# Optimization experiments

Hardware: AMD Instinct MI355X
Metric: run time of the kernel (lower is better)

## Reference

```python
import jax, jax.numpy as jnp
import numpy as np

B = 256          # batch
IMG = 28         # img_width
K = 9            # kernel_size
NUM_CLASSES = 10
NUM_ITER = 3
NUM_ROUTE = 32 * 6 * 6  # 1152


def _conv(x, w, b, stride):
    # x: [B,C,H,W], w: [O,I,K,K] (OIHW), VALID padding as in nn.Conv2d(padding=0)
    y = jax.lax.conv_general_dilated(x, w, (stride, stride), 'VALID',
                                     dimension_numbers=('NCHW', 'OIHW', 'NCHW'))
    return y + b[None, :, None, None]


def _squash(t, axis=-1):
    sq = jnp.sum(t * t, axis=axis, keepdims=True)
    return (sq / (1.0 + sq)) * t / jnp.sqrt(sq)


def setup_inputs() -> dict:
    key = jax.random.key(0)
    ks = jax.random.split(key, 10)
    rn = lambda k, s, sc=0.05: jax.random.normal(k, s, dtype=jnp.float32) * sc
    return {
        'x': jax.random.uniform(ks[0], (B, 1, IMG, IMG), dtype=jnp.float32),
        'conv1_w': rn(ks[1], (256, 1, K, K)),
        'conv1_b': jnp.zeros((256,), jnp.float32),
        # 8 primary-capsule convs of 32 channels stacked as one 256-out conv
        'prim_w': rn(ks[2], (8 * 32, 256, K, K)),
        'prim_b': jnp.zeros((8 * 32,), jnp.float32),
        # torch.randn init, std 1, shape [num_capsules, num_route_nodes, in, out]
        'route_w': jax.random.normal(ks[3], (NUM_CLASSES, NUM_ROUTE, 8, 16), dtype=jnp.float32),
        'dec_w1': rn(ks[4], (16 * NUM_CLASSES, 512)),
        'dec_b1': jnp.zeros((512,), jnp.float32),
        'dec_w2': rn(ks[5], (512, 1024)),
        'dec_b2': jnp.zeros((1024,), jnp.float32),
        'dec_w3': rn(ks[6], (1024, IMG * IMG)),
        'dec_b3': jnp.zeros((IMG * IMG,), jnp.float32),
    }


def reference(x, conv1_w, conv1_b, prim_w, prim_b, route_w,
              dec_w1, dec_b1, dec_w2, dec_b2, dec_w3, dec_b3):
    b = x.shape[0]
    # conv1 + relu: [B,256,20,20]
    h = jax.nn.relu(_conv(x, conv1_w, conv1_b, 1))
    # primary capsules: [B,8*32,6,6] -> [B,1152,8] (capsule c flattens its own 32x6x6 block)
    p = _conv(h, prim_w, prim_b, 2)
    p = p.reshape(b, 8, -1).transpose(0, 2, 1)
    p = _squash(p)  # squash over the 8-dim capsule vectors
    # priors: [10,B,1152,1,16]
    priors = jnp.einsum('bri,crio->cbro', p, route_w)[:, :, :, None, :]
    logits = jnp.zeros_like(priors)
    outputs = None
    for i in range(NUM_ITER):
        probs = jax.nn.softmax(logits, axis=2)            # over route nodes
        outputs = _squash(jnp.sum(probs * priors, axis=2, keepdims=True))  # [10,B,1,1,16]
        if i != NUM_ITER - 1:
            logits = logits + jnp.sum(priors * outputs, axis=-1, keepdims=True)
    v = outputs.reshape(NUM_CLASSES, b, 16).transpose(1, 0, 2)  # [B,10,16]
    classes = jax.nn.softmax(jnp.sqrt(jnp.sum(v * v, axis=-1)), axis=1)  # [B,10]
    # y is None path: one-hot of argmax class
    y = jax.nn.one_hot(jnp.argmax(classes, axis=1), NUM_CLASSES, dtype=v.dtype)
    masked = (v * y[:, :, None]).reshape(b, -1)  # [B,160]
    h1 = jax.nn.relu(masked @ dec_w1 + dec_b1)
    h2 = jax.nn.relu(h1 @ dec_w2 + dec_b2)
    recon = jax.nn.sigmoid(h2 @ dec_w3 + dec_b3)  # [B,784]
    return classes, recon
```

## Files before the change

### kernel.cpp

```cpp
#include <hip/hip_runtime.h>
#include <hip/hip_bf16.h>
#include <math.h>

constexpr int BB = 256;
constexpr int NCLS = 10;
constexpr int NROUTE = 1152;

typedef __attribute__((ext_vector_type(8))) short s16x8;
typedef __attribute__((ext_vector_type(4))) float f32x4;

__device__ __forceinline__ void gl16(const void* g, void* l) {
  __builtin_amdgcn_global_load_lds(
      (const __attribute__((address_space(1))) void*)g,
      (__attribute__((address_space(3))) void*)l, 16, 0, 0);
}

__global__ __launch_bounds__(256) void k_conv1b(const float* __restrict__ x,
    const float* __restrict__ w, const float* __restrict__ bias,
    __hip_bfloat16* __restrict__ hT_hi, __hip_bfloat16* __restrict__ hT_lo,
    int b0) {
  int b_l = blockIdx.x >> 2, q = blockIdx.x & 3;
  __shared__ float sx[784];
  __shared__ float sw[64 * 81];
  int t = threadIdx.x;
  for (int i = t; i < 784; i += 256) sx[i] = x[(size_t)(b0 + b_l) * 784 + i];
  for (int i = t; i < 5184; i += 256) sw[i] = w[(size_t)q * 5184 + i];
  __syncthreads();
  int oc = q * 64 + (t & 63);
  int wv = t >> 6;
  float wreg[81];
#pragma unroll
  for (int k = 0; k < 81; ++k) wreg[k] = sw[(t & 63) * 81 + k];
  float bv = bias[oc];
  for (int st = wv * 10; st < wv * 10 + 10; ++st) {
    int y = st >> 1, x0 = (st & 1) * 10;
    float acc[10];
#pragma unroll
    for (int i = 0; i < 10; ++i) acc[i] = bv;
#pragma unroll
    for (int ky = 0; ky < 9; ++ky) {
      const float* row = &sx[(y + ky) * 28 + x0];
      float rv[18];
#pragma unroll
      for (int i = 0; i < 18; ++i) rv[i] = row[i];
#pragma unroll
      for (int kx = 0; kx < 9; ++kx) {
        float wgt = wreg[ky * 9 + kx];
#pragma unroll
        for (int xi = 0; xi < 10; ++xi) acc[xi] = fmaf(rv[kx + xi], wgt, acc[xi]);
      }
    }
#pragma unroll
    for (int xi = 0; xi < 10; ++xi) {
      float av = fmaxf(acc[xi], 0.f);
      __hip_bfloat16 hi = __float2bfloat16(av);
      float lo = av - __bfloat162float(hi);
      size_t idx = ((size_t)(b_l * 400 + y * 20 + x0 + xi)) * 256 + oc;
      hT_hi[idx] = hi;
      hT_lo[idx] = __float2bfloat16(lo);
    }
  }
}

__global__ __launch_bounds__(256) void k_cvtw(const float* __restrict__ w,
    __hip_bfloat16* __restrict__ wt_hi, __hip_bfloat16* __restrict__ wt_lo) {
  int oc = blockIdx.x >> 2, icq = blockIdx.x & 3;
  __shared__ float sw[5184];
  int t = threadIdx.x;
  const float* src = w + ((size_t)oc * 256 + icq * 64) * 81;
  for (int i = t; i < 5184; i += 256) sw[i] = src[i];
  __syncthreads();
  for (int i = t; i < 5184; i += 256) {
    int tap = i >> 6, icl = i & 63;
    float v = sw[icl * 81 + tap];
    __hip_bfloat16 hi = __float2bfloat16(v);
    float lo = v - __bfloat162float(hi);
    size_t dst = (size_t)tap * 65536 + (size_t)oc * 256 + icq * 64 + icl;
    wt_hi[dst] = hi;
    wt_lo[dst] = __float2bfloat16(lo);
  }
}

constexpr int P4_BUF = 32768;

__global__ __launch_bounds__(256) void k_prim4(
    const __hip_bfloat16* __restrict__ hT_hi, const __hip_bfloat16* __restrict__ hT_lo,
    const __hip_bfloat16* __restrict__ wt_hi, const __hip_bfloat16* __restrict__ wt_lo,
    float* __restrict__ pout) {
  __shared__ __align__(16) char lds[2 * P4_BUF];
  int x = blockIdx.x & 7, g = blockIdx.x >> 3;
  int nM = (x < 4) ? 5 : 4;
  if (g >= nM * 6) return;
  int Mblk = x + (g / 6) * 8;
  int rem = g % 6;
  int kb = rem % 3, Nblk = rem / 3;
  int m0 = Mblk * 128, oc0 = Nblk * 128;
  int t = threadIdx.x, wv = t >> 6, lane = t & 63;
  int q = t & 3;
  int rA = t >> 2;
  int jswz = q ^ (rA & 3);
  size_t roA0, roA1;
  {
    int m = m0 + rA; int b = m / 36, s = m - b * 36, oy = s / 6, ox = s - oy * 6;
    roA0 = ((size_t)(b * 400 + oy * 40 + ox * 2)) * 512 + (size_t)(jswz * 16);
    m = m0 + rA + 64; b = m / 36; s = m - b * 36; oy = s / 6; ox = s - oy * 6;
    roA1 = ((size_t)(b * 400 + oy * 40 + ox * 2)) * 512 + (size_t)(jswz * 16);
  }
  size_t boB0 = ((size_t)(oc0 + rA)) * 512 + (size_t)(jswz * 16);
  size_t boB1 = ((size_t)(oc0 + rA + 64)) * 512 + (size_t)(jswz * 16);
  const char* hTh = (const char*)hT_hi;
  const char* hTl = (const char*)hT_lo;
  const char* wth = (const char*)wt_hi;
  const char* wtl = (const char*)wt_lo;

  auto stage = [&](int bufi, int s) {
    int tt = s >> 3, icc = s & 7;
    int tap = kb * 27 + tt;
    int ky = tap / 9, kx = tap - ky * 9;
    size_t offA = (size_t)((ky * 20 + kx) * 512 + icc * 64);
    size_t offB = (size_t)tap * 131072 + (size_t)(icc * 64);
    char* d = lds + bufi * P4_BUF + t * 16;
    gl16(hTh + roA0 + offA, d);
    gl16(hTh + roA1 + offA, d + 4096);
    gl16(hTl + roA0 + offA, d + 8192);
    gl16(hTl + roA1 + offA, d + 12288);
    gl16(wth + boB0 + offB, d + 16384);
    gl16(wth + boB1 + offB, d + 20480);
    gl16(wtl + boB0 + offB, d + 24576);
    gl16(wtl + boB1 + offB, d + 28672);
  };

  int wr = wv >> 1, wc = wv & 1;
  int lr = lane & 15;
  int swz16 = ((lane >> 4) ^ (lane & 3)) * 16;
  int arow[4], brow[4];
#pragma unroll
  for (int i = 0; i < 4; ++i) arow[i] = (wr * 64 + i * 16 + lr) * 64 + swz16;
#pragma unroll
  for (int j = 0; j < 4; ++j) brow[j] = 16384 + (wc * 64 + j * 16 + lr) * 64 + swz16;

  f32x4 acc[4][4];
#pragma unroll
  for (int i = 0; i < 4; ++i)
#pragma unroll
    for (int j = 0; j < 4; ++j) acc[i][j] = (f32x4){0.f, 0.f, 0.f, 0.f};

  stage(0, 0);
  __syncthreads();
#pragma unroll 1
  for (int s = 0; s < 216; ++s) {
    int cur = s & 1;
    if (s + 1 < 216) stage(cur ^ 1, s + 1);
    const char* Ab = lds + cur * P4_BUF;
    s16x8 ah[4], al[4], bh[4], bl[4];
#pragma unroll
    for (int i = 0; i < 4; ++i) {
      ah[i] = *(const s16x8*)(Ab + arow[i]);
      al[i] = *(const s16x8*)(Ab + 8192 + arow[i]);
    }
#pragma unroll
    for (int j = 0; j < 4; ++j) {
      bh[j] = *(const s16x8*)(Ab + brow[j]);
      bl[j] = *(const s16x8*)(Ab + 8192 + brow[j]);
    }
#pragma unroll
    for (int i = 0; i < 4; ++i)
#pragma unroll
      for (int j = 0; j < 4; ++j) {
        acc[i][j] = __builtin_amdgcn_mfma_f32_16x16x32_bf16(ah[i], bh[j], acc[i][j], 0, 0, 0);
        acc[i][j] = __builtin_amdgcn_mfma_f32_16x16x32_bf16(ah[i], bl[j], acc[i][j], 0, 0, 0);
        acc[i][j] = __builtin_amdgcn_mfma_f32_16x16x32_bf16(al[i], bh[j], acc[i][j], 0, 0, 0);
      }
    __syncthreads();
  }
  float* pb = pout + (size_t)kb * (4608 * 256);
#pragma unroll
  for (int i = 0; i < 4; ++i)
#pragma unroll
    for (int j = 0; j < 4; ++j) {
      int n = oc0 + wc * 64 + j * 16 + lr;
#pragma unroll
      for (int qq = 0; qq < 4; ++qq) {
        int m = m0 + wr * 64 + i * 16 + (lane >> 4) * 4 + qq;
        pb[(size_t)m * 256 + n] = acc[i][j][qq];
      }
    }
}

__global__ __launch_bounds__(256) void k_squash3(const float* __restrict__ pout,
    const float* __restrict__ bias, float* __restrict__ psT, int b0) {
  int s = blockIdx.x;
  int b_l = blockIdx.y;
  int t = threadIdx.x;
  int c32 = t & 31;
  __shared__ float ws[4][32];
  __shared__ float buf2[256];
  size_t base = ((size_t)(b_l * 36 + s)) * 256 + t;
  float val = pout[base] + pout[base + 1179648] + pout[base + 2359296] + bias[t];
  float v2 = val * val;
  v2 += __shfl_xor(v2, 32);
  int wvv = t >> 6, lane = t & 63;
  if (lane < 32) ws[wvv][lane] = v2;
  __syncthreads();
  float ss = ws[0][c32] + ws[1][c32] + ws[2][c32] + ws[3][c32];
  float sc = sqrtf(ss) / (1.f + ss);
  buf2[t] = val * sc;
  __syncthreads();
  int cc = t >> 3, jj = t & 7;
  psT[(size_t)(b0 + b_l) * 9216 + (size_t)cc * 288 + s * 8 + jj] =
      buf2[jj * 32 + cc];
}

__global__ __launch_bounds__(768) void k_route5(const float* __restrict__ psT,
    const float* __restrict__ rw, float* __restrict__ vout) {
  int c = blockIdx.x >> 8;
  int b = blockIdx.x & 255;
  int tid = threadIdx.x;
  int wave = tid >> 6, lane = tid & 63;
  int oh = lane >> 5;
  int rs = wave * 32 + (lane & 31);
  __shared__ float lredm[12];
  __shared__ float lreds[12];
  __shared__ float ored[12][2][8];
  __shared__ float osum[16];
  __shared__ float vsq[16];

  float pri[3][8];
  float lgr[3] = {0.f, 0.f, 0.f};
#pragma unroll
  for (int k = 0; k < 3; ++k)
#pragma unroll
    for (int j = 0; j < 8; ++j) pri[k][j] = 0.f;

#pragma unroll
  for (int k = 0; k < 3; ++k) {
    int r = rs + k * 384;
    const float* wr_ = &rw[((size_t)c * 1152 + r) * 128 + oh * 8];
    const float4* pp = (const float4*)&psT[((size_t)b * 1152 + r) * 8];
    float4 pa = pp[0], pb4 = pp[1];
    float ps8[8] = {pa.x, pa.y, pa.z, pa.w, pb4.x, pb4.y, pb4.z, pb4.w};
#pragma unroll
    for (int i = 0; i < 8; ++i) {
      float4 w0 = *(const float4*)&wr_[i * 16];
      float4 w1 = *(const float4*)&wr_[i * 16 + 4];
      float w8[8] = {w0.x, w0.y, w0.z, w0.w, w1.x, w1.y, w1.z, w1.w};
#pragma unroll
      for (int j = 0; j < 8; ++j) pri[k][j] = fmaf(ps8[i], w8[j], pri[k][j]);
    }
  }

  for (int it = 0; it < 3; ++it) {
    float a[8];
    if (it == 0) {
      const float invu = 1.f / 1152.f;
#pragma unroll
      for (int j = 0; j < 8; ++j)
        a[j] = (pri[0][j] + pri[1][j] + pri[2][j]) * invu;
    } else {
      float mx = fmaxf(fmaxf(lgr[0], lgr[1]), lgr[2]);
#pragma unroll
      for (int off = 16; off; off >>= 1) mx = fmaxf(mx, __shfl_xor(mx, off));
      if (lane == 0) lredm[wave] = mx;
      __syncthreads();
      mx = lredm[0];
      for (int w = 1; w < 12; ++w) mx = fmaxf(mx, lredm[w]);
      float er[3];
      float sm = 0.f;
#pragma unroll
      for (int k = 0; k < 3; ++k) {
        er[k] = expf(lgr[k] - mx);
        sm += er[k];
      }
#pragma unroll
      for (int off = 16; off; off >>= 1) sm += __shfl_xor(sm, off);
      if (lane == 0) lreds[wave] = sm;
      __syncthreads();
      float s = 0.f;
      for (int w = 0; w < 12; ++w) s += lreds[w];
      float inv = 1.f / s;
#pragma unroll
      for (int j = 0; j < 8; ++j) a[j] = 0.f;
#pragma unroll
      for (int k = 0; k < 3; ++k) {
        float p = er[k] * inv;
#pragma unroll
        for (int j = 0; j < 8; ++j) a[j] = fmaf(p, pri[k][j], a[j]);
      }
    }
#pragma unroll
    for (int off = 16; off; off >>= 1)
#pragma unroll
      for (int j = 0; j < 8; ++j) a[j] += __shfl_xor(a[j], off);
    if ((lane & 31) == 0) {
#pragma unroll
      for (int j = 0; j < 8; ++j) ored[wave][oh][j] = a[j];
    }
    __syncthreads();
    if (tid < 16) {
      float s = 0.f;
      for (int w = 0; w < 12; ++w) s += ored[w][tid >> 3][tid & 7];
      osum[tid] = s;
    }
    __syncthreads();
    if (tid < 16) {
      float sqv = 0.f;
#pragma unroll
      for (int o = 0; o < 16; ++o) sqv += osum[o] * osum[o];
      float sc = sqrtf(sqv) / (1.f + sqv);
      vsq[tid] = osum[tid] * sc;
    }
    __syncthreads();
    if (it < 2) {
      float vh[8];
#pragma unroll
      for (int j = 0; j < 8; ++j) vh[j] = vsq[oh * 8 + j];
#pragma unroll
      for (int k = 0; k < 3; ++k) {
        float d = 0.f;
#pragma unroll
        for (int j = 0; j < 8; ++j) d = fmaf(pri[k][j], vh[j], d);
        d += __shfl_xor(d, 32);
        lgr[k] += d;
      }
      __syncthreads();
    }
  }
  if (tid < 16) vout[((size_t)c * BB + b) * 16 + tid] = vsq[tid];
}

__global__ __launch_bounds__(64) void k_cls2(const float* __restrict__ v,
                                             float* __restrict__ classes,
                                             int* __restrict__ am,
                                             float* __restrict__ vsel) {
  int b = blockIdx.x;
  int t = threadIdx.x;
  __shared__ float snrm[10];
  __shared__ int samax;
  if (t < 10) {
    float sq = 0.f;
#pragma unroll
    for (int o = 0; o < 16; ++o) {
      float xx = v[(size_t)(t * BB + b) * 16 + o];
      sq += xx * xx;
    }
    snrm[t] = sqrtf(sq);
  }
  __syncthreads();
  if (t == 0) {
    int amx = 0;
    float bm = snrm[0];
    for (int cc = 1; cc < 10; ++cc)
      if (snrm[cc] > bm) { bm = snrm[cc]; amx = cc; }
    samax = amx;
    am[b] = amx;
  }
  __syncthreads();
  if (t < 10) {
    float mx = snrm[0];
    for (int cc = 1; cc < 10; ++cc) mx = fmaxf(mx, snrm[cc]);
    float sm = 0.f;
    for (int cc = 0; cc < 10; ++cc) sm += expf(snrm[cc] - mx);
    classes[b * 10 + t] = expf(snrm[t] - mx) / sm;
  }
  if (t < 16) vsel[b * 16 + t] = v[((size_t)samax * BB + b) * 16 + t];
}

__global__ __launch_bounds__(512) void k_fc1s(const float* __restrict__ vsel,
    const int* __restrict__ am, const float* __restrict__ w1,
    const float* __restrict__ b1, float* __restrict__ h1) {
  int b = blockIdx.x;
  int n = threadIdx.x;
  __shared__ float sv[16];
  __shared__ int sam;
  if (n < 16) sv[n] = vsel[b * 16 + n];
  if (n == 0) sam = am[b];
  __syncthreads();
  float acc = b1[n];
  int base = sam * 16;
#pragma unroll
  for (int i = 0; i < 16; ++i)
    acc = fmaf(sv[i], w1[(size_t)(base + i) * 512 + n], acc);
  h1[(size_t)b * 512 + n] = fmaxf(acc, 0.f);
}

template <int ACT>
__global__ __launch_bounds__(256) void k_fc32(const float* __restrict__ A,
                                              const float* __restrict__ W,
                                              const float* __restrict__ bias,
                                              float* __restrict__ O, int M,
                                              int N, int K) {
  int n0 = blockIdx.x * 32, m0 = blockIdx.y * 32;
  __shared__ float sa[32][33];
  __shared__ float sb[32][34];
  int tid = threadIdx.x, ty = tid >> 4, tx = tid & 15;
  float acc[2][2] = {};
  for (int k0 = 0; k0 < K; k0 += 32) {
    __syncthreads();
    for (int i = tid; i < 1024; i += 256) {
      int m = i >> 5, k = i & 31;
      sa[m][k] = A[(size_t)(m0 + m) * K + k0 + k];
      int kk = i >> 5, n = i & 31;
      int nn = n0 + n;
      sb[kk][n] = (nn < N) ? W[(size_t)(k0 + kk) * N + nn] : 0.f;
    }
    __syncthreads();
#pragma unroll
    for (int k = 0; k < 32; ++k) {
      float a0 = sa[ty * 2 + 0][k];
      float a1 = sa[ty * 2 + 1][k];
      float b0 = sb[k][tx * 2 + 0];
      float b1v = sb[k][tx * 2 + 1];
      acc[0][0] = fmaf(a0, b0, acc[0][0]);
      acc[0][1] = fmaf(a0, b1v, acc[0][1]);
      acc[1][0] = fmaf(a1, b0, acc[1][0]);
      acc[1][1] = fmaf(a1, b1v, acc[1][1]);
    }
  }
#pragma unroll
  for (int i = 0; i < 2; ++i) {
    int m = m0 + ty * 2 + i;
#pragma unroll
    for (int j = 0; j < 2; ++j) {
      int n = n0 + tx * 2 + j;
      if (n < N) {
        float xv = acc[i][j] + bias[n];
        if (ACT == 0)
          xv = fmaxf(xv, 0.f);
        else
          xv = 1.f / (1.f + expf(-xv));
        O[(size_t)m * N + n] = xv;
      }
    }
  }
}

extern "C" void kernel_launch(void* const* d_in, const int* in_sizes, int n_in,
                              void* d_out, int out_size, void* d_ws,
                              size_t ws_size, hipStream_t stream) {
  (void)in_sizes; (void)n_in; (void)out_size; (void)ws_size;
  const float* x       = (const float*)d_in[0];
  const float* conv1_w = (const float*)d_in[1];
  const float* conv1_b = (const float*)d_in[2];
  const float* prim_w  = (const float*)d_in[3];
  const float* prim_b  = (const float*)d_in[4];
  const float* route_w = (const float*)d_in[5];
  const float* dec_w1  = (const float*)d_in[6];
  const float* dec_b1  = (const float*)d_in[7];
  const float* dec_w2  = (const float*)d_in[8];
  const float* dec_b2  = (const float*)d_in[9];
  const float* dec_w3  = (const float*)d_in[10];
  const float* dec_b3  = (const float*)d_in[11];
  float* out = (float*)d_out;

  char* wsb = (char*)d_ws;
  __hip_bfloat16* hT_hi = (__hip_bfloat16*)(wsb);
  __hip_bfloat16* hT_lo = (__hip_bfloat16*)(wsb + 26214400);
  __hip_bfloat16* wt_hi = (__hip_bfloat16*)(wsb + 52428800);
  __hip_bfloat16* wt_lo = (__hip_bfloat16*)(wsb + 63045632);
  float* pout = (float*)(wsb + 73662464);
  float* psT  = (float*)(wsb + 87818240);
  float* v    = (float*)(wsb + 97255424);
  float* h1   = (float*)(wsb + 97419264);
  float* h2   = (float*)(wsb + 97943552);
  int*   am   = (int*)  (wsb + 98992128);
  float* vsel = (float*)(wsb + 98996224);

  k_cvtw<<<1024, 256, 0, stream>>>(prim_w, wt_hi, wt_lo);
  for (int hh = 0; hh < 2; ++hh) {
    int b0 = hh * 128;
    k_conv1b<<<512, 256, 0, stream>>>(x, conv1_w, conv1_b, hT_hi, hT_lo, b0);
    k_prim4<<<240, 256, 0, stream>>>(hT_hi, hT_lo, wt_hi, wt_lo, pout);
    k_squash3<<<dim3(36, 128), 256, 0, stream>>>(pout, prim_b, psT, b0);
  }
  k_route5<<<2560, 768, 0, stream>>>(psT, route_w, v);
  k_cls2<<<256, 64, 0, stream>>>(v, out, am, vsel);
  k_fc1s<<<256, 512, 0, stream>>>(vsel, am, dec_w1, dec_b1, h1);
  k_fc32<0><<<dim3(32, 8), 256, 0, stream>>>(h1, dec_w2, dec_b2, h2, 256, 1024, 512);
  k_fc32<1><<<dim3(25, 8), 256, 0, stream>>>(h2, dec_w3, dec_b3, out + 2560, 256, 784, 1024);
}
```

Baseline: 792.7 us.

## Replace syncthreads with fine-grained waitcnt barriers and setprio in prim GEMM loop

Rewrites the double-buffered main loop of the primary-capsule GEMM to use explicit s_waitcnt vmcnt/lgkmcnt plus s_barrier instead of full __syncthreads. This lets the next tile's global-to-LDS loads stay in flight while the current tile is read. The last iteration is peeled so the loop has no conditional stage. s_setprio is raised around the MFMA block to favor matrix issue. The risk is correctness: it assumes exactly 8 outstanding loads per stage, and a wrong count would break synchronization.

```diff
diff --git a/kernel.cpp b/kernel.cpp
--- a/kernel.cpp
+++ b/kernel.cpp
@@ -83,7 +83,7 @@
 
 constexpr int P4_BUF = 32768;
 
-__global__ __launch_bounds__(256) void k_prim4(
+__global__ __launch_bounds__(256) void k_prim5(
     const __hip_bfloat16* __restrict__ hT_hi, const __hip_bfloat16* __restrict__ hT_lo,
     const __hip_bfloat16* __restrict__ wt_hi, const __hip_bfloat16* __restrict__ wt_lo,
     float* __restrict__ pout) {
@@ -146,11 +146,18 @@
     for (int j = 0; j < 4; ++j) acc[i][j] = (f32x4){0.f, 0.f, 0.f, 0.f};
 
   stage(0, 0);
-  __syncthreads();
+  asm volatile("s_waitcnt vmcnt(0)" ::: "memory");
+  __builtin_amdgcn_s_barrier();
+  __builtin_amdgcn_sched_barrier(0);
+
 #pragma unroll 1
-  for (int s = 0; s < 216; ++s) {
+  for (int s = 0; s < 215; ++s) {
     int cur = s & 1;
-    if (s + 1 < 216) stage(cur ^ 1, s + 1);
+    stage(cur ^ 1, s + 1);
+    __builtin_amdgcn_sched_barrier(0);
+    asm volatile("s_waitcnt vmcnt(8)" ::: "memory");
+    __builtin_amdgcn_s_barrier();
+    __builtin_amdgcn_sched_barrier(0);
     const char* Ab = lds + cur * P4_BUF;
     s16x8 ah[4], al[4], bh[4], bl[4];
 #pragma unroll
@@ -163,6 +170,11 @@
       bh[j] = *(const s16x8*)(Ab + brow[j]);
       bl[j] = *(const s16x8*)(Ab + 8192 + brow[j]);
     }
+    asm volatile("s_waitcnt lgkmcnt(0)" ::: "memory");
+    __builtin_amdgcn_sched_barrier(0);
+    __builtin_amdgcn_s_barrier();
+    __builtin_amdgcn_sched_barrier(0);
+    __builtin_amdgcn_s_setprio(1);
 #pragma unroll
     for (int i = 0; i < 4; ++i)
 #pragma unroll
@@ -171,7 +183,35 @@
         acc[i][j] = __builtin_amdgcn_mfma_f32_16x16x32_bf16(ah[i], bl[j], acc[i][j], 0, 0, 0);
         acc[i][j] = __builtin_amdgcn_mfma_f32_16x16x32_bf16(al[i], bh[j], acc[i][j], 0, 0, 0);
       }
-    __syncthreads();
+    __builtin_amdgcn_s_setprio(0);
+    __builtin_amdgcn_sched_barrier(0);
+  }
+  {
+    asm volatile("s_waitcnt vmcnt(0)" ::: "memory");
+    __builtin_amdgcn_s_barrier();
+    __builtin_amdgcn_sched_barrier(0);
+    const char* Ab = lds + P4_BUF;
+    s16x8 ah[4], al[4], bh[4], bl[4];
+#pragma unroll
+    for (int i = 0; i < 4; ++i) {
+      ah[i] = *(const s16x8*)(Ab + arow[i]);
+      al[i] = *(const s16x8*)(Ab + 8192 + arow[i]);
+    }
+#pragma unroll
+    for (int j = 0; j < 4; ++j) {
+      bh[j] = *(const s16x8*)(Ab + brow[j]);
+      bl[j] = *(const s16x8*)(Ab + 8192 + brow[j]);
+    }
+    asm volatile("s_waitcnt lgkmcnt(0)" ::: "memory");
+    __builtin_amdgcn_sched_barrier(0);
+#pragma unroll
+    for (int i = 0; i < 4; ++i)
+#pragma unroll
+      for (int j = 0; j < 4; ++j) {
+        acc[i][j] = __builtin_amdgcn_mfma_f32_16x16x32_bf16(ah[i], bh[j], acc[i][j], 0, 0, 0);
+        acc[i][j] = __builtin_amdgcn_mfma_f32_16x16x32_bf16(ah[i], bl[j], acc[i][j], 0, 0, 0);
+        acc[i][j] = __builtin_amdgcn_mfma_f32_16x16x32_bf16(al[i], bh[j], acc[i][j], 0, 0, 0);
+      }
   }
   float* pb = pout + (size_t)kb * (4608 * 256);
 #pragma unroll
@@ -469,7 +509,7 @@
   for (int hh = 0; hh < 2; ++hh) {
     int b0 = hh * 128;
     k_conv1b<<<512, 256, 0, stream>>>(x, conv1_w, conv1_b, hT_hi, hT_lo, b0);
-    k_prim4<<<240, 256, 0, stream>>>(hT_hi, hT_lo, wt_hi, wt_lo, pout);
+    k_prim5<<<240, 256, 0, stream>>>(hT_hi, hT_lo, wt_hi, wt_lo, pout);
     k_squash3<<<dim3(36, 128), 256, 0, stream>>>(pout, prim_b, psT, b0);
   }
   k_route5<<<2560, 768, 0, stream>>>(psT, route_w, v);
```

Result: slower. 885.5 us (+11.7%).

## Use 512-thread blocks and register-staged prefetch in primary capsule GEMM

Applied to the files above, without the earlier changes.

The primary-capsule GEMM kernel moves from 4 to 8 waves per block, so each wave computes a 64x32 tile instead of 64x64. Tile staging switches from direct global-to-LDS loads to loading into registers first and writing to LDS after the MFMA block. The aim is more latency hiding through more waves and overlap of the next tile's global loads with compute. In exchange each wave re-reads its A fragments from LDS more often relative to the math it does, and the extra staging registers may limit occupancy.

```diff
diff --git a/kernel.cpp b/kernel.cpp
--- a/kernel.cpp
+++ b/kernel.cpp
@@ -8,12 +8,6 @@
 
 typedef __attribute__((ext_vector_type(8))) short s16x8;
 typedef __attribute__((ext_vector_type(4))) float f32x4;
-
-__device__ __forceinline__ void gl16(const void* g, void* l) {
-  __builtin_amdgcn_global_load_lds(
-      (const __attribute__((address_space(1))) void*)g,
-      (__attribute__((address_space(3))) void*)l, 16, 0, 0);
-}
 
 __global__ __launch_bounds__(256) void k_conv1b(const float* __restrict__ x,
     const float* __restrict__ w, const float* __restrict__ bias,
@@ -81,13 +75,13 @@
   }
 }
 
-constexpr int P4_BUF = 32768;
-
-__global__ __launch_bounds__(256) void k_prim4(
+constexpr int P6_BUF = 32768;
+
+__global__ __launch_bounds__(512, 2) void k_prim6(
     const __hip_bfloat16* __restrict__ hT_hi, const __hip_bfloat16* __restrict__ hT_lo,
     const __hip_bfloat16* __restrict__ wt_hi, const __hip_bfloat16* __restrict__ wt_lo,
     float* __restrict__ pout) {
-  __shared__ __align__(16) char lds[2 * P4_BUF];
+  __shared__ __align__(16) char lds[2 * P6_BUF];
   int x = blockIdx.x & 7, g = blockIdx.x >> 3;
   int nM = (x < 4) ? 5 : 4;
   if (g >= nM * 6) return;
@@ -96,89 +90,92 @@
   int kb = rem % 3, Nblk = rem / 3;
   int m0 = Mblk * 128, oc0 = Nblk * 128;
   int t = threadIdx.x, wv = t >> 6, lane = t & 63;
-  int q = t & 3;
+  int jswz = (t & 3) ^ ((t >> 2) & 3);
   int rA = t >> 2;
-  int jswz = q ^ (rA & 3);
-  size_t roA0, roA1;
+  size_t roA;
   {
-    int m = m0 + rA; int b = m / 36, s = m - b * 36, oy = s / 6, ox = s - oy * 6;
-    roA0 = ((size_t)(b * 400 + oy * 40 + ox * 2)) * 512 + (size_t)(jswz * 16);
-    m = m0 + rA + 64; b = m / 36; s = m - b * 36; oy = s / 6; ox = s - oy * 6;
-    roA1 = ((size_t)(b * 400 + oy * 40 + ox * 2)) * 512 + (size_t)(jswz * 16);
-  }
-  size_t boB0 = ((size_t)(oc0 + rA)) * 512 + (size_t)(jswz * 16);
-  size_t boB1 = ((size_t)(oc0 + rA + 64)) * 512 + (size_t)(jswz * 16);
+    int m = m0 + rA;
+    int b = m / 36, s = m - b * 36, oy = s / 6, ox = s - oy * 6;
+    roA = ((size_t)(b * 400 + oy * 40 + ox * 2)) * 512 + (size_t)(jswz * 16);
+  }
+  size_t boB = ((size_t)(oc0 + rA)) * 512 + (size_t)(jswz * 16);
   const char* hTh = (const char*)hT_hi;
   const char* hTl = (const char*)hT_lo;
   const char* wth = (const char*)wt_hi;
   const char* wtl = (const char*)wt_lo;
 
-  auto stage = [&](int bufi, int s) {
+  int4 rah, ral, rbh, rbl;
+  auto loadregs = [&](int s) {
     int tt = s >> 3, icc = s & 7;
     int tap = kb * 27 + tt;
     int ky = tap / 9, kx = tap - ky * 9;
     size_t offA = (size_t)((ky * 20 + kx) * 512 + icc * 64);
     size_t offB = (size_t)tap * 131072 + (size_t)(icc * 64);
-    char* d = lds + bufi * P4_BUF + t * 16;
-    gl16(hTh + roA0 + offA, d);
-    gl16(hTh + roA1 + offA, d + 4096);
-    gl16(hTl + roA0 + offA, d + 8192);
-    gl16(hTl + roA1 + offA, d + 12288);
-    gl16(wth + boB0 + offB, d + 16384);
-    gl16(wth + boB1 + offB, d + 20480);
-    gl16(wtl + boB0 + offB, d + 24576);
-    gl16(wtl + boB1 + offB, d + 28672);
+    rah = *(const int4*)(hTh + roA + offA);
+    ral = *(const int4*)(hTl + roA + offA);
+    rbh = *(const int4*)(wth + boB + offB);
+    rbl = *(const int4*)(wtl + boB + offB);
   };
-
-  int wr = wv >> 1, wc = wv & 1;
+  auto writeregs = [&](int bufi) {
+    char* d = lds + bufi * P6_BUF + t * 16;
+    *(int4*)(d) = rah;
+    *(int4*)(d + 8192) = ral;
+    *(int4*)(d + 16384) = rbh;
+    *(int4*)(d + 24576) = rbl;
+  };
+
+  int wr = wv >> 2, wc = wv & 3;
   int lr = lane & 15;
   int swz16 = ((lane >> 4) ^ (lane & 3)) * 16;
-  int arow[4], brow[4];
+  int arow[4], brow[2];
 #pragma unroll
   for (int i = 0; i < 4; ++i) arow[i] = (wr * 64 + i * 16 + lr) * 64 + swz16;
 #pragma unroll
-  for (int j = 0; j < 4; ++j) brow[j] = 16384 + (wc * 64 + j * 16 + lr) * 64 + swz16;
-
-  f32x4 acc[4][4];
+  for (int j = 0; j < 2; ++j) brow[j] = 16384 + (wc * 32 + j * 16 + lr) * 64 + swz16;
+
+  f32x4 acc[4][2];
 #pragma unroll
   for (int i = 0; i < 4; ++i)
 #pragma unroll
-    for (int j = 0; j < 4; ++j) acc[i][j] = (f32x4){0.f, 0.f, 0.f, 0.f};
-
-  stage(0, 0);
-  __syncthreads();
+    for (int j = 0; j < 2; ++j) acc[i][j] = (f32x4){0.f, 0.f, 0.f, 0.f};
+
+  loadregs(0);
+  writeregs(0);
+  __syncthreads();
+
 #pragma unroll 1
   for (int s = 0; s < 216; ++s) {
     int cur = s & 1;
-    if (s + 1 < 216) stage(cur ^ 1, s + 1);
-    const char* Ab = lds + cur * P4_BUF;
-    s16x8 ah[4], al[4], bh[4], bl[4];
+    if (s < 215) loadregs(s + 1);
+    const char* Ab = lds + cur * P6_BUF;
+    s16x8 ah[4], al[4], bh[2], bl[2];
 #pragma unroll
     for (int i = 0; i < 4; ++i) {
       ah[i] = *(const s16x8*)(Ab + arow[i]);
       al[i] = *(const s16x8*)(Ab + 8192 + arow[i]);
     }
 #pragma unroll
-    for (int j = 0; j < 4; ++j) {
+    for (int j = 0; j < 2; ++j) {
       bh[j] = *(const s16x8*)(Ab + brow[j]);
       bl[j] = *(const s16x8*)(Ab + 8192 + brow[j]);
     }
 #pragma unroll
     for (int i = 0; i < 4; ++i)
 #pragma unroll
-      for (int j = 0; j < 4; ++j) {
+      for (int j = 0; j < 2; ++j) {
         acc[i][j] = __builtin_amdgcn_mfma_f32_16x16x32_bf16(ah[i], bh[j], acc[i][j], 0, 0, 0);
         acc[i][j] = __builtin_amdgcn_mfma_f32_16x16x32_bf16(ah[i], bl[j], acc[i][j], 0, 0, 0);
         acc[i][j] = __builtin_amdgcn_mfma_f32_16x16x32_bf16(al[i], bh[j], acc[i][j], 0, 0, 0);
       }
+    if (s < 215) writeregs(cur ^ 1);
     __syncthreads();
   }
   float* pb = pout + (size_t)kb * (4608 * 256);
 #pragma unroll
   for (int i = 0; i < 4; ++i)
 #pragma unroll
-    for (int j = 0; j < 4; ++j) {
-      int n = oc0 + wc * 64 + j * 16 + lr;
+    for (int j = 0; j < 2; ++j) {
+      int n = oc0 + wc * 32 + j * 16 + lr;
 #pragma unroll
       for (int qq = 0; qq < 4; ++qq) {
         int m = m0 + wr * 64 + i * 16 + (lane >> 4) * 4 + qq;
@@ -469,7 +466,7 @@
   for (int hh = 0; hh < 2; ++hh) {
     int b0 = hh * 128;
     k_conv1b<<<512, 256, 0, stream>>>(x, conv1_w, conv1_b, hT_hi, hT_lo, b0);
-    k_prim4<<<240, 256, 0, stream>>>(hT_hi, hT_lo, wt_hi, wt_lo, pout);
+    k_prim6<<<240, 512, 0, stream>>>(hT_hi, hT_lo, wt_hi, wt_lo, pout);
     k_squash3<<<dim3(36, 128), 256, 0, stream>>>(pout, prim_b, psT, b0);
   }
   k_route5<<<2560, 768, 0, stream>>>(psT, route_w, v);
```

After: 769.9 us. 2.9% less time.
